# Performance work log

Measured on AMD Instinct MI355X. Metric: run time of the kernel, lower is better.

The kernel has to match this reference:

```python
import jax, jax.numpy as jnp
import numpy as np

N = 20000       # nodes
E = 100000      # edges
STEPS = 4
ND = 128        # node feature dim
ED = 128        # edge feature dim
NIN = 128       # node input dim
EIN = 291       # edge input dim (2 + 17*17)
H = 64          # mpn edge-mlp hidden


def _lin(x, w, b):
    return x @ w + b


def setup_inputs():
    key = jax.random.key(0)
    ks = jax.random.split(key, 16)

    def w(k, i, o):
        return (jax.random.normal(k, (i, o), jnp.float32) / np.float32(np.sqrt(i)))

    d = {}
    d["x"] = jax.random.normal(ks[0], (N, NIN), jnp.float32)
    d["edge_attr"] = jax.random.normal(ks[1], (E, EIN), jnp.float32)
    d["edge_index"] = jax.random.randint(ks[2], (2, E), 0, N, jnp.int32)
    # node embedding MLP: NIN -> 128 -> ND (ReLU between, none after last)
    d["new0"] = w(ks[3], NIN, 128); d["neb0"] = jnp.zeros(128, jnp.float32)
    d["new1"] = w(ks[4], 128, ND); d["neb1"] = jnp.zeros(ND, jnp.float32)
    # edge embedding MLP: EIN -> 64 -> ED
    d["eew0"] = w(ks[5], EIN, 64); d["eeb0"] = jnp.zeros(64, jnp.float32)
    d["eew1"] = w(ks[6], 64, ED); d["eeb1"] = jnp.zeros(ED, jnp.float32)
    # MPN edge MLP (skip=True): 2*(2*ND) + 2*ED = 768 -> 64 -> ED, ReLU after each
    d["mew0"] = w(ks[7], 4 * ND + 2 * ED, H); d["meb0"] = jnp.zeros(H, jnp.float32)
    d["mew1"] = w(ks[8], H, ED); d["meb1"] = jnp.zeros(ED, jnp.float32)
    # MPN node MLP: 2*ND + ED = 384 -> ND, ReLU
    d["mnw0"] = w(ks[9], 2 * ND + ED, ND); d["mnb0"] = jnp.zeros(ND, jnp.float32)
    # classification MLP: ED -> 64 -> 32 -> 1
    d["cw0"] = w(ks[10], ED, 64); d["cb0"] = jnp.zeros(64, jnp.float32)
    d["cw1"] = w(ks[11], 64, 32); d["cb1"] = jnp.zeros(32, jnp.float32)
    d["cw2"] = w(ks[12], 32, 1); d["cb2"] = jnp.zeros(1, jnp.float32)
    return d


def reference(x, edge_attr, edge_index,
              new0, neb0, new1, neb1,
              eew0, eeb0, eew1, eeb1,
              mew0, meb0, mew1, meb1,
              mnw0, mnb0,
              cw0, cb0, cw1, cb1, cw2, cb2):
    relu = jax.nn.relu
    j, i = edge_index[0], edge_index[1]  # j: source, i: target

    nf = _lin(relu(_lin(x, new0, neb0)), new1, neb1)          # [N, ND]
    ef = _lin(relu(_lin(edge_attr, eew0, eeb0)), eew1, eeb1)  # [E, ED]
    nf0, ef0 = nf, ef

    for _ in range(STEPS):
        # skip connections: concat initial features
        nfc = jnp.concatenate([nf0, nf], axis=1)  # [N, 2*ND]
        efc = jnp.concatenate([ef0, ef], axis=1)  # [E, 2*ED]
        x_i = nfc[i]  # [E, 2*ND] target
        x_j = nfc[j]  # [E, 2*ND] source
        # edge update MLP (ReLU after both layers)
        h = relu(_lin(jnp.concatenate([x_i, x_j, efc], axis=1), mew0, meb0))
        ef = relu(_lin(h, mew1, meb1))  # [E, ED]
        # message: mlp_node([x_i, edge_attr_new]) aggregated at target i
        msg = relu(_lin(jnp.concatenate([x_i, ef], axis=1), mnw0, mnb0))  # [E, ND]
        nf = jax.ops.segment_sum(msg, i, num_segments=N)  # [N, ND]

    out = relu(_lin(ef, cw0, cb0))
    out = relu(_lin(out, cw1, cb1))
    out = _lin(out, cw2, cb2)  # [E, 1]
    return out
```

## Files before the change

kernel.cpp:

```cpp
#include <hip/hip_runtime.h>
#include <hip/hip_bf16.h>

#define ND 128
#define ED 128
#define NIN 128
#define EIN 291
#define KPAD 320
#define HH 64
#define TM 32
#define TS 64
#define GSE 768
#define MAXGE 3

typedef __attribute__((ext_vector_type(8))) short short8;
typedef __attribute__((ext_vector_type(4))) float float4_;

__device__ __forceinline__ unsigned short f2bf(float f)
{
    union { float f; unsigned u; } v; v.f = f;
    unsigned u = v.u;
    unsigned r = (u + 0x7FFFu + ((u >> 16) & 1u)) >> 16;
    return (unsigned short)r;
}
__device__ __forceinline__ float bf2f(unsigned short s)
{
    union { unsigned u; float f; } v; v.u = ((unsigned)s) << 16;
    return v.f;
}

template<int T, int KC, int K>
__device__ __forceinline__ void stage_frags(const unsigned short* __restrict__ src,
                                            unsigned short* __restrict__ wreg,
                                            int t, int k0)
{
    constexpr int TOT = T * KC * 64;
#pragma unroll
    for (int it = 0; it < TOT / 256; it++) {
        int idx = it * 256 + t;
        int f = idx >> 6, l = idx & 63;
        int col = (f / KC) * 16 + (l & 15);
        int k = (f % KC) * 32 + ((l >> 4) * 8);
        *(short8*)&wreg[idx * 8] = *(const short8*)&src[(size_t)col * K + k0 + k];
    }
}
#define FRAG(wreg, f, lane) (*(const short8*)&(wreg)[(((f) << 6) + (lane)) * 8])

__global__ __launch_bounds__(256) void zero_k(float* __restrict__ p, int n4)
{
    int idx = blockIdx.x * 256 + threadIdx.x;
    if (idx < n4) ((float4*)p)[idx] = make_float4(0.f, 0.f, 0.f, 0.f);
}

__global__ __launch_bounds__(256) void hist_k(const int* __restrict__ tgti,
                                              int* __restrict__ deg, int E)
{
    int e = blockIdx.x * 256 + threadIdx.x;
    if (e < E) atomicAdd(&deg[tgti[e]], 1);
}

__global__ __launch_bounds__(256) void scan_k(const int* __restrict__ deg,
                                              int* __restrict__ row_ptr,
                                              int* __restrict__ cursor, int N, int E)
{
    __shared__ int part[256];
    const int t = threadIdx.x;
    const int chunk = (N + 255) / 256;
    const int base = t * chunk;
    int s = 0;
    for (int k = 0; k < chunk; k++) { int idx = base + k; if (idx < N) s += deg[idx]; }
    part[t] = s;
    __syncthreads();
    for (int off = 1; off < 256; off <<= 1) {
        int v = (t >= off) ? part[t - off] : 0;
        __syncthreads();
        part[t] += v;
        __syncthreads();
    }
    int run = (t == 0) ? 0 : part[t - 1];
    for (int k = 0; k < chunk; k++) {
        int idx = base + k;
        if (idx < N) { row_ptr[idx] = run; cursor[idx] = run; run += deg[idx]; }
    }
    if (t == 255) row_ptr[N] = E;
}

__global__ __launch_bounds__(256) void scatter_k(const int* __restrict__ srcj,
                                                 const int* __restrict__ tgti,
                                                 int* __restrict__ cursor,
                                                 int* __restrict__ csr_eid,
                                                 int* __restrict__ srcp,
                                                 int* __restrict__ tgtp, int E)
{
    int e = blockIdx.x * 256 + threadIdx.x;
    if (e < E) {
        int tg = tgti[e];
        int p = atomicAdd(&cursor[tg], 1);
        csr_eid[p] = e;
        srcp[p] = srcj[e];
        tgtp[p] = tg;
    }
}

__global__ __launch_bounds__(256) void fixup_k(const int* __restrict__ row_ptr,
                                               float* __restrict__ nfx,
                                               unsigned short* __restrict__ nf_out, int N)
{
    int n = blockIdx.x * 2 + (threadIdx.x >> 7);
    int c = threadIdx.x & 127;
    if (n >= N) return;
    int beg = row_ptr[n], end = row_ptr[n + 1];
    if (beg == end) { nf_out[(size_t)n * ND + c] = 0; return; }
    if ((beg >> 5) != ((end - 1) >> 5)) {
        size_t idx = (size_t)n * ND + c;
        nf_out[idx] = f2bf(nfx[idx]);
        nfx[idx] = 0.f;
    }
}

__global__ __launch_bounds__(256) void wprep_k(
    const float* __restrict__ mew0, const float* __restrict__ mew1, const float* __restrict__ mnw0,
    const float* __restrict__ eew0, const float* __restrict__ eew1, const float* __restrict__ cw0,
    const float* __restrict__ new0, const float* __restrict__ new1,
    unsigned short* __restrict__ w0T, unsigned short* __restrict__ w1T,
    unsigned short* __restrict__ wmT, unsigned short* __restrict__ w0eT,
    unsigned short* __restrict__ w1eT, unsigned short* __restrict__ cw0T,
    unsigned short* __restrict__ w0nT, unsigned short* __restrict__ w1nT,
    int* __restrict__ deg, int N)
{
    int idx = blockIdx.x * 256 + threadIdx.x;
    if (idx < 49152) {
        int c = idx / 768, k = idx % 768;
        w0T[idx] = f2bf(mew0[k * 64 + c]);
    } else if (idx < 57344) {
        int j = idx - 49152; int c = j / 64, k = j % 64;
        w1T[j] = f2bf(mew1[k * 128 + c]);
    } else if (idx < 106496) {
        int j = idx - 57344; int c = j / 384, k = j % 384;
        wmT[j] = f2bf(mnw0[k * 128 + c]);
    } else if (idx < 126976) {
        int j = idx - 106496; int c = j / KPAD, k = j % KPAD;
        w0eT[j] = (k < EIN) ? f2bf(eew0[k * 64 + c]) : (unsigned short)0;
    } else if (idx < 135168) {
        int j = idx - 126976; int c = j / 64, k = j % 64;
        w1eT[j] = f2bf(eew1[k * 128 + c]);
    } else if (idx < 143360) {
        int j = idx - 135168; int c = j / 128, k = j % 128;
        cw0T[j] = f2bf(cw0[k * 64 + c]);
    } else if (idx < 159744) {
        int j = idx - 143360; int c = j / 128, k = j % 128;
        w0nT[j] = f2bf(new0[k * 128 + c]);
    } else if (idx < 176128) {
        int j = idx - 159744; int c = j / 128, k = j % 128;
        w1nT[j] = f2bf(new1[k * 128 + c]);
    } else if (idx < 176128 + N) {
        deg[idx - 176128] = 0;
    }
}

__global__ __launch_bounds__(256, 3) void embed_k(
    const float* __restrict__ ea, const int* __restrict__ csr_eid,
    const unsigned short* __restrict__ w0eT, const float* __restrict__ eb0,
    const unsigned short* __restrict__ w1eT, const float* __restrict__ eb1,
    unsigned short* __restrict__ ef0_bf, unsigned short* __restrict__ ef_bf,
    int E, int ntiles,
    const float* __restrict__ x,
    const unsigned short* __restrict__ w0nT, const float* __restrict__ nb0,
    const unsigned short* __restrict__ w1nT, const float* __restrict__ nb1,
    unsigned short* __restrict__ nf0_bf, unsigned short* __restrict__ nf_bf, int N)
{
    __shared__ unsigned short smem[22656];
    const int t = threadIdx.x;
    const int w = t >> 6, lane = t & 63, quad = lane >> 4, n16 = lane & 15;

    if (blockIdx.x < GSE) {
        unsigned short* w0reg = smem;
        unsigned short* w1reg = smem + 10240;
        unsigned short* hsl   = smem + 18432;

        stage_frags<8, 2, 64>(w1eT, w1reg, t, 0);

        int ng = 0;
        int tile[MAXGE];
#pragma unroll
        for (int g = 0; g < MAXGE; g++) {
            int tl = blockIdx.x + g * GSE;
            if (tl < ntiles) { tile[g] = tl; ng = g + 1; }
            else tile[g] = 0;
        }

        float4_ accL[MAXGE][4];
#pragma unroll
        for (int g = 0; g < MAXGE; g++)
#pragma unroll
            for (int q = 0; q < 4; q++) accL[g][q] = (float4_){0.f, 0.f, 0.f, 0.f};

#pragma unroll
        for (int hf = 0; hf < 2; hf++) {
            __syncthreads();
            stage_frags<4, 5, KPAD>(w0eT, w0reg, t, hf * 160);
            __syncthreads();
#pragma unroll
            for (int g = 0; g < MAXGE; g++) {
                if (g < ng) {
                    int p = tile[g] * 64 + w * 16 + n16; if (p >= E) p = E - 1;
                    const float* src = ea + (size_t)csr_eid[p] * EIN;
#pragma unroll
                    for (int kc = 0; kc < 5; kc++) {
                        int k = hf * 160 + kc * 32 + quad * 8;
                        union { short8 s; uint4 u; } av;
                        if (k + 8 <= EIN) {
                            float4 v0 = *(const float4*)(src + k);
                            float4 v1 = *(const float4*)(src + k + 4);
                            av.u.x = (unsigned)f2bf(v0.x) | ((unsigned)f2bf(v0.y) << 16);
                            av.u.y = (unsigned)f2bf(v0.z) | ((unsigned)f2bf(v0.w) << 16);
                            av.u.z = (unsigned)f2bf(v1.x) | ((unsigned)f2bf(v1.y) << 16);
                            av.u.w = (unsigned)f2bf(v1.z) | ((unsigned)f2bf(v1.w) << 16);
                        } else {
                            unsigned short vv[8];
#pragma unroll
                            for (int j = 0; j < 8; j++)
                                vv[j] = (k + j < EIN) ? f2bf(src[k + j]) : (unsigned short)0;
                            av.u.x = (unsigned)vv[0] | ((unsigned)vv[1] << 16);
                            av.u.y = (unsigned)vv[2] | ((unsigned)vv[3] << 16);
                            av.u.z = (unsigned)vv[4] | ((unsigned)vv[5] << 16);
                            av.u.w = (unsigned)vv[6] | ((unsigned)vv[7] << 16);
                        }
#pragma unroll
                        for (int tt = 0; tt < 4; tt++) {
                            short8 b = FRAG(w0reg, tt * 5 + kc, lane);
                            accL[g][tt] = __builtin_amdgcn_mfma_f32_16x16x32_bf16(av.s, b, accL[g][tt], 0, 0, 0);
                        }
                    }
                }
            }
        }

#pragma unroll
        for (int g = 0; g < MAXGE; g++) {
            if (g < ng) {
#pragma unroll
                for (int tt = 0; tt < 4; tt++) {
                    int c = tt * 16 + n16;
                    float bias = eb0[c];
#pragma unroll
                    for (int r4 = 0; r4 < 4; r4++)
                        hsl[w * 1056 + (quad * 4 + r4) * 66 + c] = f2bf(fmaxf(accL[g][tt][r4] + bias, 0.f));
                }
                float4_ acc2[8];
#pragma unroll
                for (int q = 0; q < 8; q++) acc2[q] = (float4_){0.f, 0.f, 0.f, 0.f};
#pragma unroll
                for (int kc = 0; kc < 2; kc++) {
                    short8 a2 = *(const short8*)&hsl[w * 1056 + n16 * 66 + kc * 32 + quad * 8];
#pragma unroll
                    for (int tt = 0; tt < 8; tt++)
                        acc2[tt] = __builtin_amdgcn_mfma_f32_16x16x32_bf16(
                            a2, FRAG(w1reg, tt * 2 + kc, lane), acc2[tt], 0, 0, 0);
                }
#pragma unroll
                for (int tt = 0; tt < 8; tt++) {
                    int c = tt * 16 + n16;
                    float bias = eb1[c];
#pragma unroll
                    for (int r4 = 0; r4 < 4; r4++) {
                        int p = tile[g] * 64 + w * 16 + quad * 4 + r4;
                        if (p < E) {
                            unsigned short v = f2bf(acc2[tt][r4] + bias);
                            ef0_bf[(size_t)p * ED + c] = v;
                            ef_bf[(size_t)p * ED + c] = v;
                        }
                    }
                }
            }
        }
    } else {
        unsigned short* wreg = smem;
        unsigned short* xin  = smem + 8192;
        unsigned short* h_bf = smem + 12352;
        const int n0 = (blockIdx.x - GSE) * TM;

#pragma unroll
        for (int it = 0; it < 4; it++) {
            int idx = it * 256 + t;
            int r = idx >> 5, c4 = idx & 31;
            int node = n0 + r; if (node >= N) node = N - 1;
            float4 v = *(const float4*)(x + (size_t)node * NIN + c4 * 4);
            unsigned lo = (unsigned)f2bf(v.x) | ((unsigned)f2bf(v.y) << 16);
            unsigned hi = (unsigned)f2bf(v.z) | ((unsigned)f2bf(v.w) << 16);
            *(uint2*)&xin[r * 130 + c4 * 4] = make_uint2(lo, hi);
        }

        const int m = w & 1, nh = w >> 1;

        float4_ acc[4];
#pragma unroll
        for (int q = 0; q < 4; q++) acc[q] = (float4_){0.f, 0.f, 0.f, 0.f};
#pragma unroll
        for (int hf = 0; hf < 2; hf++) {
            stage_frags<8, 2, 128>(w0nT, wreg, t, hf * 64);
            __syncthreads();
#pragma unroll
            for (int kc = 0; kc < 2; kc++) {
                short8 a = *(const short8*)&xin[(m * 16 + n16) * 130 + hf * 64 + kc * 32 + quad * 8];
#pragma unroll
                for (int tt = 0; tt < 4; tt++) {
                    short8 b = FRAG(wreg, (nh * 4 + tt) * 2 + kc, lane);
                    acc[tt] = __builtin_amdgcn_mfma_f32_16x16x32_bf16(a, b, acc[tt], 0, 0, 0);
                }
            }
            __syncthreads();
        }
#pragma unroll
        for (int tt = 0; tt < 4; tt++) {
            int c = nh * 64 + tt * 16 + n16;
            float bias = nb0[c];
#pragma unroll
            for (int r4 = 0; r4 < 4; r4++)
                h_bf[(m * 16 + quad * 4 + r4) * 130 + c] = f2bf(fmaxf(acc[tt][r4] + bias, 0.f));
        }
        __syncthreads();

        float4_ acc2[4];
#pragma unroll
        for (int q = 0; q < 4; q++) acc2[q] = (float4_){0.f, 0.f, 0.f, 0.f};
#pragma unroll
        for (int hf = 0; hf < 2; hf++) {
            stage_frags<8, 2, 128>(w1nT, wreg, t, hf * 64);
            __syncthreads();
#pragma unroll
            for (int kc = 0; kc < 2; kc++) {
                short8 a = *(const short8*)&h_bf[(m * 16 + n16) * 130 + hf * 64 + kc * 32 + quad * 8];
#pragma unroll
                for (int tt = 0; tt < 4; tt++) {
                    short8 b = FRAG(wreg, (nh * 4 + tt) * 2 + kc, lane);
                    acc2[tt] = __builtin_amdgcn_mfma_f32_16x16x32_bf16(a, b, acc2[tt], 0, 0, 0);
                }
            }
            __syncthreads();
        }
#pragma unroll
        for (int tt = 0; tt < 4; tt++) {
            int c = nh * 64 + tt * 16 + n16;
            float bias = nb1[c];
#pragma unroll
            for (int r4 = 0; r4 < 4; r4++) {
                int row = m * 16 + quad * 4 + r4;
                int node = n0 + row;
                if (node < N) {
                    unsigned short v = f2bf(acc2[tt][r4] + bias);
                    nf0_bf[(size_t)node * ND + c] = v;
                    nf_bf[(size_t)node * ND + c] = v;
                }
            }
        }
    }
}

__global__ __launch_bounds__(256, 4) void edge_step_k(
    const int* __restrict__ srcp, const int* __restrict__ tgtp,
    const unsigned short* __restrict__ nf0_bf, const unsigned short* __restrict__ nf_in,
    const unsigned short* __restrict__ ef0_bf, unsigned short* __restrict__ ef_bf,
    unsigned short* __restrict__ nf_out, float* __restrict__ nfx,
    const unsigned short* __restrict__ w0T, const float* __restrict__ meb0,
    const unsigned short* __restrict__ w1T, const float* __restrict__ meb1,
    const unsigned short* __restrict__ wmT, const float* __restrict__ mnb0,
    int E, int wmsg)
{
    const int t = threadIdx.x;
    const int e0 = blockIdx.x * TS;
    __shared__ unsigned short wreg[8192];
    __shared__ unsigned short hef[4][2080];

    const int w = t >> 6, lane = t & 63, quad = lane >> 4, n16 = lane & 15;
    int ec = e0 + w * 16 + n16; if (ec >= E) ec = E - 1;
    const int ti = tgtp[ec], sj = srcp[ec];

    const unsigned short* pA[6] = {
        nf0_bf + (size_t)ti * ND + quad * 8,
        nf_in  + (size_t)ti * ND + quad * 8,
        nf0_bf + (size_t)sj * ND + quad * 8,
        nf_in  + (size_t)sj * ND + quad * 8,
        ef0_bf + (size_t)ec * ED + quad * 8,
        ef_bf  + (size_t)ec * ED + quad * 8 };

    float4_ accL[4];
#pragma unroll
    for (int q = 0; q < 4; q++) accL[q] = (float4_){0.f, 0.f, 0.f, 0.f};
#pragma unroll
    for (int hf = 0; hf < 6; hf++) {
        short8 a4[4];
#pragma unroll
        for (int q2 = 0; q2 < 4; q2++)
            a4[q2] = *(const short8*)(pA[hf] + q2 * 32);
        stage_frags<4, 4, 768>(w0T, wreg, t, hf * 128);
        __syncthreads();
#pragma unroll
        for (int kc = 0; kc < 4; kc++) {
#pragma unroll
            for (int tt = 0; tt < 4; tt++) {
                short8 b = FRAG(wreg, tt * 4 + kc, lane);
                accL[tt] = __builtin_amdgcn_mfma_f32_16x16x32_bf16(a4[kc], b, accL[tt], 0, 0, 0);
            }
        }
        __syncthreads();
    }

#pragma unroll
    for (int tt = 0; tt < 4; tt++) {
        int c = tt * 16 + n16;
        float bias = meb0[c];
#pragma unroll
        for (int r4 = 0; r4 < 4; r4++)
            hef[w][(quad * 4 + r4) * 66 + c] = f2bf(fmaxf(accL[tt][r4] + bias, 0.f));
    }

    stage_frags<8, 2, 64>(w1T, wreg, t, 0);
    __syncthreads();
    {
        float4_ acc[8];
#pragma unroll
        for (int q = 0; q < 8; q++) acc[q] = (float4_){0.f, 0.f, 0.f, 0.f};
#pragma unroll
        for (int kc = 0; kc < 2; kc++) {
            short8 a = *(const short8*)&hef[w][n16 * 66 + kc * 32 + quad * 8];
#pragma unroll
            for (int tt = 0; tt < 8; tt++) {
                short8 b = FRAG(wreg, tt * 2 + kc, lane);
                acc[tt] = __builtin_amdgcn_mfma_f32_16x16x32_bf16(a, b, acc[tt], 0, 0, 0);
            }
        }
#pragma unroll
        for (int tt = 0; tt < 8; tt++) {
            int c = tt * 16 + n16;
            float bias = meb1[c];
#pragma unroll
            for (int r4 = 0; r4 < 4; r4++) {
                int row = quad * 4 + r4;
                unsigned short v = f2bf(fmaxf(acc[tt][r4] + bias, 0.f));
                hef[w][row * 130 + c] = v;
                int e = e0 + w * 16 + row;
                if (e < E) ef_bf[(size_t)e * ED + c] = v;
            }
        }
    }
    __syncthreads();

    if (wmsg) {
        float4_ accM[8];
#pragma unroll
        for (int q = 0; q < 8; q++) accM[q] = (float4_){0.f, 0.f, 0.f, 0.f};
#pragma unroll
        for (int j = 0; j < 6; j++) {
            short8 a2[2];
#pragma unroll
            for (int kc = 0; kc < 2; kc++) {
                int kk = j * 2 + kc;
                if (kk < 8) a2[kc] = *(const short8*)(pA[kk >> 2] + (kk & 3) * 32);
                else        a2[kc] = *(const short8*)&hef[w][n16 * 130 + (kk - 8) * 32 + quad * 8];
            }
            stage_frags<8, 2, 384>(wmT, wreg, t, j * 64);
            __syncthreads();
#pragma unroll
            for (int kc = 0; kc < 2; kc++) {
#pragma unroll
                for (int tt = 0; tt < 8; tt++) {
                    short8 b = FRAG(wreg, tt * 2 + kc, lane);
                    accM[tt] = __builtin_amdgcn_mfma_f32_16x16x32_bf16(a2[kc], b, accM[tt], 0, 0, 0);
                }
            }
            __syncthreads();
        }

#pragma unroll
        for (int tt = 0; tt < 8; tt++) {
            int c = tt * 16 + n16;
            float bias = mnb0[c];
#pragma unroll
            for (int r4 = 0; r4 < 4; r4++) {
                int row = w * 16 + quad * 4 + r4;
                wreg[row * 128 + c] = f2bf(fmaxf(accM[tt][r4] + bias, 0.f));
            }
        }
        int* tg = (int*)&hef[0][0];
        if (t < 66) {
            int p = e0 - 1 + t;
            tg[t] = (p >= 0 && p < E) ? tgtp[p] : -1;
        }
        __syncthreads();
        {
            int c = t & 127, half = t >> 7;
            int r0 = half * 32;
            float acc = 0.f;
            int rs = 0;
            for (int r = 0; r < 32; r++) {
                int p = e0 + r0 + r;
                if (p >= E) break;
                int n = tg[r0 + r + 1];
                acc += bf2f(wreg[(r0 + r) * 128 + c]);
                bool end_here = (tg[r0 + r + 2] != n);
                if (end_here) {
                    bool beg_in = (rs > 0) || (tg[r0] != n);
                    if (beg_in) nf_out[(size_t)n * ND + c] = f2bf(acc);
                    else        atomicAdd(&nfx[(size_t)n * ND + c], acc);
                    acc = 0.f; rs = r + 1;
                } else if (r == 31) {
                    atomicAdd(&nfx[(size_t)n * ND + c], acc);
                }
            }
        }
    }
}

__global__ __launch_bounds__(256) void classify_k(
    const unsigned short* __restrict__ ef_bf, const int* __restrict__ csr_eid,
    const unsigned short* __restrict__ cw0T, const float* __restrict__ cb0,
    const float* __restrict__ cw1, const float* __restrict__ cb1,
    const float* __restrict__ cw2, const float* __restrict__ cb2,
    float* __restrict__ out, int E)
{
    const int t = threadIdx.x;
    const int e0 = blockIdx.x * TM;
    __shared__ unsigned short h0_bf[TM][66];
    __shared__ float h1[TM][33];

    const int w = t >> 6, lane = t & 63, quad = lane >> 4, n16 = lane & 15;
    const int m = w & 1;
    const int erow = m * 16 + n16;
    int ec = e0 + erow; if (ec >= E) ec = E - 1;
    const unsigned short* pa = ef_bf + (size_t)ec * ED + quad * 8;

    {
        const int cb = (w >> 1) * 32;
        float4_ acc0 = {0.f, 0.f, 0.f, 0.f}, acc1 = acc0;
        const unsigned short* b0p = cw0T + (size_t)(cb + n16) * 128 + quad * 8;
        const unsigned short* b1p = b0p + (size_t)16 * 128;
#pragma unroll
        for (int kc = 0; kc < 4; kc++) {
            short8 a  = *(const short8*)(pa + kc * 32);
            short8 bb0 = *(const short8*)(b0p + kc * 32);
            short8 bb1 = *(const short8*)(b1p + kc * 32);
            acc0 = __builtin_amdgcn_mfma_f32_16x16x32_bf16(a, bb0, acc0, 0, 0, 0);
            acc1 = __builtin_amdgcn_mfma_f32_16x16x32_bf16(a, bb1, acc1, 0, 0, 0);
        }
#pragma unroll
        for (int t2 = 0; t2 < 2; t2++) {
            int c = cb + t2 * 16 + n16;
            float bias = cb0[c];
            float4_ ac = t2 ? acc1 : acc0;
#pragma unroll
            for (int r4 = 0; r4 < 4; r4++)
                h0_bf[m * 16 + quad * 4 + r4][c] = f2bf(fmaxf(ac[r4] + bias, 0.f));
        }
    }
    __syncthreads();

    {
        int c = t & 31;
        int rbase = (t >> 5) * 4;
#pragma unroll
        for (int q = 0; q < 4; q++) {
            int r = rbase + q;
            float acc = cb1[c];
#pragma unroll 8
            for (int k = 0; k < 64; k++) acc += bf2f(h0_bf[r][k]) * cw1[k * 32 + c];
            h1[r][c] = fmaxf(acc, 0.f);
        }
    }
    __syncthreads();

    if (t < TM) {
        int p = e0 + t;
        if (p < E) {
            float a = cb2[0];
#pragma unroll
            for (int k = 0; k < 32; k++) a += h1[t][k] * cw2[k];
            out[csr_eid[p]] = a;
        }
    }
}

extern "C" void kernel_launch(void* const* d_in, const int* in_sizes, int n_in,
                              void* d_out, int out_size, void* d_ws, size_t ws_size,
                              hipStream_t stream)
{
    const float* x    = (const float*)d_in[0];
    const float* ea   = (const float*)d_in[1];
    const int*   eidx = (const int*)d_in[2];
    const float* new0 = (const float*)d_in[3];  const float* neb0 = (const float*)d_in[4];
    const float* new1 = (const float*)d_in[5];  const float* neb1 = (const float*)d_in[6];
    const float* eew0 = (const float*)d_in[7];  const float* eeb0 = (const float*)d_in[8];
    const float* eew1 = (const float*)d_in[9];  const float* eeb1 = (const float*)d_in[10];
    const float* mew0 = (const float*)d_in[11]; const float* meb0 = (const float*)d_in[12];
    const float* mew1 = (const float*)d_in[13]; const float* meb1 = (const float*)d_in[14];
    const float* mnw0 = (const float*)d_in[15]; const float* mnb0 = (const float*)d_in[16];
    const float* cw0  = (const float*)d_in[17]; const float* cb0  = (const float*)d_in[18];
    const float* cw1  = (const float*)d_in[19]; const float* cb1  = (const float*)d_in[20];
    const float* cw2  = (const float*)d_in[21]; const float* cb2  = (const float*)d_in[22];

    const int N = in_sizes[0] / NIN;
    const int E = in_sizes[2] / 2;
    const int* srcj = eidx;
    const int* tgti = eidx + E;

    char* wsb = (char*)d_ws;
    unsigned short* nf0_bf = (unsigned short*)wsb;
    unsigned short* nfA    = nf0_bf + (size_t)N * ND;
    unsigned short* ef0_bf = nfA + (size_t)N * ND;
    unsigned short* ef_bf  = ef0_bf + (size_t)E * ED;
    unsigned short* slot   = ef_bf + (size_t)E * ED;
    unsigned short* nfB    = slot;
    float*          nfx    = (float*)(slot + (size_t)N * ND);
    unsigned short* w0T  = slot + (size_t)E * ND;
    unsigned short* w1T  = w0T + 49152;
    unsigned short* wmT  = w1T + 8192;
    unsigned short* w0eT = wmT + 49152;
    unsigned short* w1eT = w0eT + 64 * KPAD;
    unsigned short* cw0T = w1eT + 8192;
    unsigned short* w0nT = cw0T + 8192;
    unsigned short* w1nT = w0nT + 16384;
    int* deg     = (int*)(w1nT + 16384);
    int* cursor  = deg + N;
    int* row_ptr = cursor + N;
    int* csr_eid = row_ptr + (N + 4);
    int* srcp    = csr_eid + E;
    int* tgtp    = srcp + E;

    const int eblocks32 = (E + TM - 1) / TM;
    const int nblocks32 = (N + TM - 1) / TM;
    const int ntiles64 = (E + 63) / 64;

    wprep_k<<<(176128 + N + 255) / 256, 256, 0, stream>>>(mew0, mew1, mnw0, eew0, eew1, cw0,
                                                          new0, new1,
                                                          w0T, w1T, wmT, w0eT, w1eT, cw0T,
                                                          w0nT, w1nT, deg, N);

    hist_k<<<(E + 255) / 256, 256, 0, stream>>>(tgti, deg, E);
    scan_k<<<1, 256, 0, stream>>>(deg, row_ptr, cursor, N, E);
    scatter_k<<<(E + 255) / 256, 256, 0, stream>>>(srcj, tgti, cursor, csr_eid, srcp, tgtp, E);

    zero_k<<<((N * ND) / 4 + 255) / 256, 256, 0, stream>>>(nfx, (N * ND) / 4);

    embed_k<<<GSE + nblocks32, 256, 0, stream>>>(ea, csr_eid, w0eT, eeb0, w1eT, eeb1,
                                                 ef0_bf, ef_bf, E, ntiles64,
                                                 x, w0nT, neb0, w1nT, neb1,
                                                 nf0_bf, nfA, N);

    unsigned short* nfR = nfA;
    unsigned short* nfW = nfB;
    for (int s = 0; s < 4; s++) {
        edge_step_k<<<ntiles64, 256, 0, stream>>>(srcp, tgtp, nf0_bf, nfR,
                                                  ef0_bf, ef_bf, nfW, nfx,
                                                  w0T, meb0, w1T, meb1, wmT, mnb0,
                                                  E, (s < 3) ? 1 : 0);
        if (s < 3) {
            fixup_k<<<(N + 1) / 2, 256, 0, stream>>>(row_ptr, nfx, nfW, N);
            unsigned short* tmp = nfR; nfR = nfW; nfW = tmp;
        }
    }

    classify_k<<<eblocks32, 256, 0, stream>>>(ef_bf, csr_eid, cw0T, cb0, cw1, cb1, cw2, cb2,
                                              (float*)d_out, E);
}
```

Baseline: 645.2 us.

## Fuse message-passing steps, fixups and classifier into one cooperative persistent kernel

Replaces the per-step edge_step/fixup launches and the final classify launch with a single cooperative kernel that loops over tiles with a grid-stride loop and uses grid.sync between phases. The zeroing of the node accumulator buffer is folded into the weight-prep kernel, which removes one more launch. The aim is to cut launch overhead and inter-kernel gaps. In exchange, the fixed grid of 1024 blocks must stay co-resident, and each block now handles several tiles serially, which may hurt load balance and latency hiding. If the cooperative launch fails, the code falls back to the original launch sequence.

```diff
diff --git a/kernel.cpp b/kernel.cpp
--- a/kernel.cpp
+++ b/kernel.cpp
@@ -1,5 +1,8 @@
 #include <hip/hip_runtime.h>
 #include <hip/hip_bf16.h>
+#include <hip/hip_cooperative_groups.h>
+
+namespace cg = cooperative_groups;
 
 #define ND 128
 #define ED 128
@@ -11,6 +14,7 @@
 #define TS 64
 #define GSE 768
 #define MAXGE 3
+#define CGRID 1024
 
 typedef __attribute__((ext_vector_type(8))) short short8;
 typedef __attribute__((ext_vector_type(4))) float float4_;
@@ -44,12 +48,6 @@
     }
 }
 #define FRAG(wreg, f, lane) (*(const short8*)&(wreg)[(((f) << 6) + (lane)) * 8])
-
-__global__ __launch_bounds__(256) void zero_k(float* __restrict__ p, int n4)
-{
-    int idx = blockIdx.x * 256 + threadIdx.x;
-    if (idx < n4) ((float4*)p)[idx] = make_float4(0.f, 0.f, 0.f, 0.f);
-}
 
 __global__ __launch_bounds__(256) void hist_k(const int* __restrict__ tgti,
                                               int* __restrict__ deg, int E)
@@ -125,7 +123,7 @@
     unsigned short* __restrict__ wmT, unsigned short* __restrict__ w0eT,
     unsigned short* __restrict__ w1eT, unsigned short* __restrict__ cw0T,
     unsigned short* __restrict__ w0nT, unsigned short* __restrict__ w1nT,
-    int* __restrict__ deg, int N)
+    int* __restrict__ deg, float* __restrict__ nfx, int N)
 {
     int idx = blockIdx.x * 256 + threadIdx.x;
     if (idx < 49152) {
@@ -154,6 +152,8 @@
         w1nT[j] = f2bf(new1[k * 128 + c]);
     } else if (idx < 176128 + N) {
         deg[idx - 176128] = 0;
+    } else if (idx < 176128 + N + (N * ND) / 4) {
+        ((float4*)nfx)[idx - 176128 - N] = make_float4(0.f, 0.f, 0.f, 0.f);
     }
 }
 
@@ -356,7 +356,8 @@
     }
 }
 
-__global__ __launch_bounds__(256, 4) void edge_step_k(
+__device__ __forceinline__ void step_tile_body(
+    int tile, int E, int wmsg,
     const int* __restrict__ srcp, const int* __restrict__ tgtp,
     const unsigned short* __restrict__ nf0_bf, const unsigned short* __restrict__ nf_in,
     const unsigned short* __restrict__ ef0_bf, unsigned short* __restrict__ ef_bf,
@@ -364,16 +365,13 @@
     const unsigned short* __restrict__ w0T, const float* __restrict__ meb0,
     const unsigned short* __restrict__ w1T, const float* __restrict__ meb1,
     const unsigned short* __restrict__ wmT, const float* __restrict__ mnb0,
-    int E, int wmsg)
-{
-    const int t = threadIdx.x;
-    const int e0 = blockIdx.x * TS;
-    __shared__ unsigned short wreg[8192];
-    __shared__ unsigned short hef[4][2080];
-
-    const int w = t >> 6, lane = t & 63, quad = lane >> 4, n16 = lane & 15;
+    unsigned short* __restrict__ wreg, unsigned short* __restrict__ hef,
+    int t, int w, int lane, int quad, int n16)
+{
+    const int e0 = tile * TS;
     int ec = e0 + w * 16 + n16; if (ec >= E) ec = E - 1;
     const int ti = tgtp[ec], sj = srcp[ec];
+    unsigned short* hw = hef + w * 2080;
 
     const unsigned short* pA[6] = {
         nf0_bf + (size_t)ti * ND + quad * 8,
@@ -411,7 +409,7 @@
         float bias = meb0[c];
 #pragma unroll
         for (int r4 = 0; r4 < 4; r4++)
-            hef[w][(quad * 4 + r4) * 66 + c] = f2bf(fmaxf(accL[tt][r4] + bias, 0.f));
+            hw[(quad * 4 + r4) * 66 + c] = f2bf(fmaxf(accL[tt][r4] + bias, 0.f));
     }
 
     stage_frags<8, 2, 64>(w1T, wreg, t, 0);
@@ -422,7 +420,7 @@
         for (int q = 0; q < 8; q++) acc[q] = (float4_){0.f, 0.f, 0.f, 0.f};
 #pragma unroll
         for (int kc = 0; kc < 2; kc++) {
-            short8 a = *(const short8*)&hef[w][n16 * 66 + kc * 32 + quad * 8];
+            short8 a = *(const short8*)&hw[n16 * 66 + kc * 32 + quad * 8];
 #pragma unroll
             for (int tt = 0; tt < 8; tt++) {
                 short8 b = FRAG(wreg, tt * 2 + kc, lane);
@@ -437,7 +435,7 @@
             for (int r4 = 0; r4 < 4; r4++) {
                 int row = quad * 4 + r4;
                 unsigned short v = f2bf(fmaxf(acc[tt][r4] + bias, 0.f));
-                hef[w][row * 130 + c] = v;
+                hw[row * 130 + c] = v;
                 int e = e0 + w * 16 + row;
                 if (e < E) ef_bf[(size_t)e * ED + c] = v;
             }
@@ -456,7 +454,7 @@
             for (int kc = 0; kc < 2; kc++) {
                 int kk = j * 2 + kc;
                 if (kk < 8) a2[kc] = *(const short8*)(pA[kk >> 2] + (kk & 3) * 32);
-                else        a2[kc] = *(const short8*)&hef[w][n16 * 130 + (kk - 8) * 32 + quad * 8];
+                else        a2[kc] = *(const short8*)&hw[n16 * 130 + (kk - 8) * 32 + quad * 8];
             }
             stage_frags<8, 2, 384>(wmT, wreg, t, j * 64);
             __syncthreads();
@@ -481,7 +479,7 @@
                 wreg[row * 128 + c] = f2bf(fmaxf(accM[tt][r4] + bias, 0.f));
             }
         }
-        int* tg = (int*)&hef[0][0];
+        int* tg = (int*)hef;
         if (t < 66) {
             int p = e0 - 1 + t;
             tg[t] = (p >= 0 && p < E) ? tgtp[p] : -1;
@@ -511,6 +509,141 @@
     }
 }
 
+__global__ __launch_bounds__(256, 4) void mpn_fused_k(
+    const int* __restrict__ srcp, const int* __restrict__ tgtp,
+    const int* __restrict__ row_ptr, const int* __restrict__ csr_eid,
+    const unsigned short* __restrict__ nf0_bf,
+    unsigned short* __restrict__ nfA, unsigned short* __restrict__ nfB,
+    const unsigned short* __restrict__ ef0_bf, unsigned short* __restrict__ ef_bf,
+    float* __restrict__ nfx,
+    const unsigned short* __restrict__ w0T, const float* __restrict__ meb0,
+    const unsigned short* __restrict__ w1T, const float* __restrict__ meb1,
+    const unsigned short* __restrict__ wmT, const float* __restrict__ mnb0,
+    const unsigned short* __restrict__ cw0T, const float* __restrict__ cb0,
+    const float* __restrict__ cw1, const float* __restrict__ cb1,
+    const float* __restrict__ cw2, const float* __restrict__ cb2,
+    float* __restrict__ out,
+    int E, int N, int ntiles)
+{
+    cg::grid_group grid = cg::this_grid();
+    __shared__ unsigned short smem[16512];
+    unsigned short* wreg = smem;
+    unsigned short* hef  = smem + 8192;
+
+    const int t = threadIdx.x;
+    const int w = t >> 6, lane = t & 63, quad = lane >> 4, n16 = lane & 15;
+
+    const unsigned short* nfR = nfA;
+    unsigned short* nfW = nfB;
+
+    for (int s = 0; s < 4; s++) {
+        const int wmsg = (s < 3) ? 1 : 0;
+        for (int tile = blockIdx.x; tile < ntiles; tile += (int)gridDim.x) {
+            step_tile_body(tile, E, wmsg, srcp, tgtp, nf0_bf, nfR,
+                           ef0_bf, ef_bf, nfW, nfx,
+                           w0T, meb0, w1T, meb1, wmT, mnb0,
+                           wreg, hef, t, w, lane, quad, n16);
+            __syncthreads();
+        }
+        __threadfence();
+        grid.sync();
+        if (wmsg) {
+            for (int base = blockIdx.x * 2; base < N; base += (int)gridDim.x * 2) {
+                int n = base + (t >> 7);
+                int c = t & 127;
+                if (n < N) {
+                    int beg = row_ptr[n], end = row_ptr[n + 1];
+                    if (beg == end) nfW[(size_t)n * ND + c] = 0;
+                    else if ((beg >> 5) != ((end - 1) >> 5)) {
+                        size_t idx = (size_t)n * ND + c;
+                        nfW[idx] = f2bf(nfx[idx]);
+                        nfx[idx] = 0.f;
+                    }
+                }
+            }
+            __threadfence();
+            grid.sync();
+            unsigned short* tmp = (unsigned short*)nfR; nfR = nfW; nfW = tmp;
+        }
+    }
+
+    unsigned short* h0_bf = smem;
+    float* h1 = (float*)(smem + 2112);
+    const int eblocks = (E + TM - 1) / TM;
+    const int m = w & 1;
+    for (int eb = blockIdx.x; eb < eblocks; eb += (int)gridDim.x) {
+        const int e0c = eb * TM;
+        int ec = e0c + m * 16 + n16; if (ec >= E) ec = E - 1;
+        const unsigned short* pa = ef_bf + (size_t)ec * ED + quad * 8;
+        {
+            const int cb = (w >> 1) * 32;
+            float4_ acc0 = {0.f, 0.f, 0.f, 0.f}, acc1 = acc0;
+            const unsigned short* b0p = cw0T + (size_t)(cb + n16) * 128 + quad * 8;
+            const unsigned short* b1p = b0p + (size_t)16 * 128;
+#pragma unroll
+            for (int kc = 0; kc < 4; kc++) {
+                short8 a  = *(const short8*)(pa + kc * 32);
+                short8 bb0 = *(const short8*)(b0p + kc * 32);
+                short8 bb1 = *(const short8*)(b1p + kc * 32);
+                acc0 = __builtin_amdgcn_mfma_f32_16x16x32_bf16(a, bb0, acc0, 0, 0, 0);
+                acc1 = __builtin_amdgcn_mfma_f32_16x16x32_bf16(a, bb1, acc1, 0, 0, 0);
+            }
+#pragma unroll
+            for (int t2 = 0; t2 < 2; t2++) {
+                int c = cb + t2 * 16 + n16;
+                float bias = cb0[c];
+                float4_ ac = t2 ? acc1 : acc0;
+#pragma unroll
+                for (int r4 = 0; r4 < 4; r4++)
+                    h0_bf[(m * 16 + quad * 4 + r4) * 66 + c] = f2bf(fmaxf(ac[r4] + bias, 0.f));
+            }
+        }
+        __syncthreads();
+        {
+            int c = t & 31;
+            int rbase = (t >> 5) * 4;
+#pragma unroll
+            for (int q = 0; q < 4; q++) {
+                int r = rbase + q;
+                float acc = cb1[c];
+#pragma unroll 8
+                for (int k = 0; k < 64; k++) acc += bf2f(h0_bf[r * 66 + k]) * cw1[k * 32 + c];
+                h1[r * 33 + c] = fmaxf(acc, 0.f);
+            }
+        }
+        __syncthreads();
+        if (t < TM) {
+            int p = e0c + t;
+            if (p < E) {
+                float a = cb2[0];
+#pragma unroll
+                for (int k = 0; k < 32; k++) a += h1[t * 33 + k] * cw2[k];
+                out[csr_eid[p]] = a;
+            }
+        }
+        __syncthreads();
+    }
+}
+
+__global__ __launch_bounds__(256, 4) void edge_step_k(
+    const int* __restrict__ srcp, const int* __restrict__ tgtp,
+    const unsigned short* __restrict__ nf0_bf, const unsigned short* __restrict__ nf_in,
+    const unsigned short* __restrict__ ef0_bf, unsigned short* __restrict__ ef_bf,
+    unsigned short* __restrict__ nf_out, float* __restrict__ nfx,
+    const unsigned short* __restrict__ w0T, const float* __restrict__ meb0,
+    const unsigned short* __restrict__ w1T, const float* __restrict__ meb1,
+    const unsigned short* __restrict__ wmT, const float* __restrict__ mnb0,
+    int E, int wmsg)
+{
+    __shared__ unsigned short smem[16512];
+    const int t = threadIdx.x;
+    const int w = t >> 6, lane = t & 63, quad = lane >> 4, n16 = lane & 15;
+    step_tile_body(blockIdx.x, E, wmsg, srcp, tgtp, nf0_bf, nf_in,
+                   ef0_bf, ef_bf, nf_out, nfx,
+                   w0T, meb0, w1T, meb1, wmT, mnb0,
+                   smem, smem + 8192, t, w, lane, quad, n16);
+}
+
 __global__ __launch_bounds__(256) void classify_k(
     const unsigned short* __restrict__ ef_bf, const int* __restrict__ csr_eid,
     const unsigned short* __restrict__ cw0T, const float* __restrict__ cb0,
@@ -525,8 +658,7 @@
 
     const int w = t >> 6, lane = t & 63, quad = lane >> 4, n16 = lane & 15;
     const int m = w & 1;
-    const int erow = m * 16 + n16;
-    int ec = e0 + erow; if (ec >= E) ec = E - 1;
+    int ec = e0 + m * 16 + n16; if (ec >= E) ec = E - 1;
     const unsigned short* pa = ef_bf + (size_t)ec * ED + quad * 8;
 
     {
@@ -629,35 +761,50 @@
     const int nblocks32 = (N + TM - 1) / TM;
     const int ntiles64 = (E + 63) / 64;
 
-    wprep_k<<<(176128 + N + 255) / 256, 256, 0, stream>>>(mew0, mew1, mnw0, eew0, eew1, cw0,
-                                                          new0, new1,
-                                                          w0T, w1T, wmT, w0eT, w1eT, cw0T,
-                                                          w0nT, w1nT, deg, N);
+    const int wprep_items = 176128 + N + (N * ND) / 4;
+    wprep_k<<<(wprep_items + 255) / 256, 256, 0, stream>>>(mew0, mew1, mnw0, eew0, eew1, cw0,
+                                                           new0, new1,
+                                                           w0T, w1T, wmT, w0eT, w1eT, cw0T,
+                                                           w0nT, w1nT, deg, nfx, N);
 
     hist_k<<<(E + 255) / 256, 256, 0, stream>>>(tgti, deg, E);
     scan_k<<<1, 256, 0, stream>>>(deg, row_ptr, cursor, N, E);
     scatter_k<<<(E + 255) / 256, 256, 0, stream>>>(srcj, tgti, cursor, csr_eid, srcp, tgtp, E);
-
-    zero_k<<<((N * ND) / 4 + 255) / 256, 256, 0, stream>>>(nfx, (N * ND) / 4);
 
     embed_k<<<GSE + nblocks32, 256, 0, stream>>>(ea, csr_eid, w0eT, eeb0, w1eT, eeb1,
                                                  ef0_bf, ef_bf, E, ntiles64,
                                                  x, w0nT, neb0, w1nT, neb1,
                                                  nf0_bf, nfA, N);
 
-    unsigned short* nfR = nfA;
-    unsigned short* nfW = nfB;
-    for (int s = 0; s < 4; s++) {
-        edge_step_k<<<ntiles64, 256, 0, stream>>>(srcp, tgtp, nf0_bf, nfR,
-                                                  ef0_bf, ef_bf, nfW, nfx,
-                                                  w0T, meb0, w1T, meb1, wmT, mnb0,
-                                                  E, (s < 3) ? 1 : 0);
-        if (s < 3) {
-            fixup_k<<<(N + 1) / 2, 256, 0, stream>>>(row_ptr, nfx, nfW, N);
-            unsigned short* tmp = nfR; nfR = nfW; nfW = tmp;
-        }
-    }
-
-    classify_k<<<eblocks32, 256, 0, stream>>>(ef_bf, csr_eid, cw0T, cb0, cw1, cb1, cw2, cb2,
-                                              (float*)d_out, E);
-}
+    {
+        float* outp = (float*)d_out;
+        int E_ = E, N_ = N, nt_ = ntiles64;
+        void* kargs[] = {
+            (void*)&srcp, (void*)&tgtp, (void*)&row_ptr, (void*)&csr_eid,
+            (void*)&nf0_bf, (void*)&nfA, (void*)&nfB, (void*)&ef0_bf, (void*)&ef_bf,
+            (void*)&nfx, (void*)&w0T, (void*)&meb0, (void*)&w1T, (void*)&meb1,
+            (void*)&wmT, (void*)&mnb0, (void*)&cw0T, (void*)&cb0, (void*)&cw1,
+            (void*)&cb1, (void*)&cw2, (void*)&cb2, (void*)&outp,
+            (void*)&E_, (void*)&N_, (void*)&nt_ };
+        hipError_t err = hipLaunchCooperativeKernel((void*)mpn_fused_k,
+                                                    dim3(CGRID), dim3(256),
+                                                    kargs, 0, stream);
+        if (err != hipSuccess) {
+            unsigned short* nfR = nfA;
+            unsigned short* nfW = nfB;
+            for (int s = 0; s < 4; s++) {
+                edge_step_k<<<ntiles64, 256, 0, stream>>>(srcp, tgtp, nf0_bf, nfR,
+                                                          ef0_bf, ef_bf, nfW, nfx,
+                                                          w0T, meb0, w1T, meb1, wmT, mnb0,
+                                                          E, (s < 3) ? 1 : 0);
+                if (s < 3) {
+                    fixup_k<<<(N + 1) / 2, 256, 0, stream>>>(row_ptr, nfx, nfW, N);
+                    unsigned short* tmp = nfR; nfR = nfW; nfW = tmp;
+                }
+            }
+            classify_k<<<eblocks32, 256, 0, stream>>>(ef_bf, csr_eid, cw0T, cb0,
+                                                      cw1, cb1, cw2, cb2,
+                                                      (float*)d_out, E);
+        }
+    }
+}
```

New measurement: 2.218 ms. 244% more time.
